# Performance work log

Measured on AMD Instinct MI355X. Metric: run time of the kernel, lower is better.

Reference implementation:

```python
import jax, jax.numpy as jnp
import numpy as np

H = 1024
V_IN = 32000
V_OUT = 32000
T = 2048
BOS, EOS = 1, 2
MAX_STEPS = 50


def setup_inputs() -> dict:
    key = jax.random.key(0)
    ks = jax.random.split(key, 10)
    def n(k, shape, scale=0.05):
        return jax.random.normal(k, shape, jnp.float32) * scale
    return {
        "src_ids": jax.random.randint(ks[0], (T,), 3, V_IN),
        "embed_input": n(ks[1], (V_IN, H), 0.1),
        "We_ih": n(ks[2], (4 * H, H)),
        "We_hh": n(ks[3], (4 * H, H)),
        "be": jnp.zeros((4 * H,), jnp.float32),
        "embed_target": n(ks[4], (V_OUT, H), 0.1),
        "Wd_ih": n(ks[5], (4 * H, H)),
        "Wd_hh": n(ks[6], (4 * H, H)),
        "bd": jnp.zeros((4 * H,), jnp.float32),
        "W_attn": n(ks[7], (H, 2 * H)),
        "b_attn": jnp.zeros((H,), jnp.float32),
        "W_out": n(ks[8], (V_OUT, H)),
        "b_out": jnp.zeros((V_OUT,), jnp.float32),
    }


def _lstm_cell(x, h, c, W_ih, W_hh, b):
    # torch LSTMCell gate order: i, f, g, o (b = b_ih + b_hh folded)
    g = W_ih @ x + W_hh @ h + b  # [4H]
    i, f, gg, o = jnp.split(g, 4)
    i = jax.nn.sigmoid(i)
    f = jax.nn.sigmoid(f)
    o = jax.nn.sigmoid(o)
    gg = jnp.tanh(gg)
    c2 = f * c + i * gg
    return o * jnp.tanh(c2), c2


def reference(src_ids, embed_input, We_ih, We_hh, be, embed_target,
              Wd_ih, Wd_hh, bd, W_attn, b_attn, W_out, b_out):
    # ---- encoder: token-wise LSTMCell scan (batch 1, state squeezed to [H]) ----
    emb = embed_input[src_ids]  # [T, H] gather (unknown-word fallback handled by in-range ids)
    h0 = jnp.zeros((H,), jnp.float32)

    def enc_step(carry, x):
        h, c = carry
        h, c = _lstm_cell(x, h, c, We_ih, We_hh, be)
        return (h, c), h

    (hT, cT), hs = jax.lax.scan(enc_step, (h0, h0), emb)  # hs: [T, H]

    # ---- greedy decoder with dot attention, fixed 50 steps + done mask ----
    def dec_step(carry, _):
        wid, ht, ct, done = carry
        x = embed_target[wid]
        ht, ct = _lstm_cell(x, ht, ct, Wd_ih, Wd_hh, bd)
        a = jax.nn.softmax(hs @ ht)          # [T] attention over encoder states
        d = a @ hs                           # [H] context
        ht_new = jnp.tanh(W_attn @ jnp.concatenate([d, ht]) + b_attn)
        logits = W_out @ ht_new + b_out      # [V_OUT]; softmax before argmax is monotone -> skip
        nid = jnp.argmax(logits).astype(wid.dtype)
        tok = jnp.where(done, 0, nid)        # pad after <eos>
        out_logits = jnp.where(done, 0.0, logits)
        done2 = done | (nid == EOS)
        return (nid, ht, ct, done2), (tok, out_logits)

    init = (jnp.asarray(BOS, src_ids.dtype), hT, cT, jnp.asarray(False))
    _, (tokens, logits) = jax.lax.scan(dec_step, init, None, length=MAX_STEPS)
    return tokens, logits  # [50], [50, V_OUT]
```

## Files before the change

### kernel.cpp

```cpp
#include <hip/hip_runtime.h>
#include <hip/hip_cooperative_groups.h>
#include <math.h>

#define HD     1024
#define TLEN   2048
#define G4H    4096
#define VOUTN  32000
#define NSTEP  50
#define BOS_ID 1
#define EOS_ID 2

#define NBLK   256
#define NTHR   256
#define JPB    (HD / NBLK)
#define TPB    (TLEN / NBLK)
#define NBLK_L 500
#define RPW_L  16

#define ENBLK 64
#define ENTHR 1024
#define EJPB  (HD / ENBLK)

#define SENTINEL 0xFFFFFFFFu

#define OFF_GX   ((size_t)0)
#define OFF_HS   (OFF_GX + (size_t)TLEN * G4H)
#define OFF_HD   (OFF_HS + (size_t)(TLEN + 1) * HD)
#define OFF_SC   (OFF_HD + 2 * HD)
#define OFF_DC   (OFF_SC + TLEN)
#define OFF_HTN  (OFF_DC + HD)
#define OFF_BMV  (OFF_HTN + HD)
#define OFF_BMI  (OFF_BMV + 512)
#define OFF_CT   (OFF_BMI + 512)
#define OFF_ST   (OFF_CT + HD)
#define OFF_HST  (OFF_ST + 64)
#define WS_NEED_HST ((OFF_HST + (size_t)HD * TLEN) * sizeof(float))

#define DEV_SCOPE __HIP_MEMORY_SCOPE_AGENT

__device__ __forceinline__ float dload(const float* p) {
    return __hip_atomic_load(p, __ATOMIC_RELAXED, DEV_SCOPE);
}
__device__ __forceinline__ void dstore(float* p, float v) {
    __hip_atomic_store(p, v, __ATOMIC_RELAXED, DEV_SCOPE);
}

__global__ __launch_bounds__(256) void fill_sentinel(float* __restrict__ hsrow1)
{
    const size_t i = ((size_t)blockIdx.x * 256 + threadIdx.x) * 4;
    uint4 v = make_uint4(SENTINEL, SENTINEL, SENTINEL, SENTINEL);
    *(uint4*)(hsrow1 + i) = v;
}

__global__ __launch_bounds__(256) void gx_gemm(
    const int* __restrict__ src_ids,
    const float* __restrict__ emb,
    const float* __restrict__ Wih,
    const float* __restrict__ be,
    float* __restrict__ Gx)
{
    __shared__ float As[128][17];
    __shared__ float Bs[128][17];
    __shared__ int   sid[128];

    const int tid = threadIdx.x;
    const int t0 = blockIdx.x * 128;
    const int r0 = blockIdx.y * 128;

    if (tid < 128) sid[tid] = src_ids[t0 + tid];
    __syncthreads();

    const int tx = tid & 15;
    const int ty = tid >> 4;
    const int lrow = tid >> 1;
    const int lk   = (tid & 1) * 8;

    float acc[8][8];
#pragma unroll
    for (int i = 0; i < 8; ++i)
#pragma unroll
        for (int j = 0; j < 8; ++j) acc[i][j] = 0.f;

    for (int k0 = 0; k0 < HD; k0 += 16) {
        {
            const float* xa = emb + (size_t)sid[lrow] * HD + k0 + lk;
            float4 v0 = *(const float4*)xa;
            float4 v1 = *(const float4*)(xa + 4);
            As[lrow][lk + 0] = v0.x; As[lrow][lk + 1] = v0.y;
            As[lrow][lk + 2] = v0.z; As[lrow][lk + 3] = v0.w;
            As[lrow][lk + 4] = v1.x; As[lrow][lk + 5] = v1.y;
            As[lrow][lk + 6] = v1.z; As[lrow][lk + 7] = v1.w;
            const float* wb = Wih + (size_t)(r0 + lrow) * HD + k0 + lk;
            float4 w0 = *(const float4*)wb;
            float4 w1 = *(const float4*)(wb + 4);
            Bs[lrow][lk + 0] = w0.x; Bs[lrow][lk + 1] = w0.y;
            Bs[lrow][lk + 2] = w0.z; Bs[lrow][lk + 3] = w0.w;
            Bs[lrow][lk + 4] = w1.x; Bs[lrow][lk + 5] = w1.y;
            Bs[lrow][lk + 6] = w1.z; Bs[lrow][lk + 7] = w1.w;
        }
        __syncthreads();
#pragma unroll
        for (int kk = 0; kk < 16; ++kk) {
            float a[8], bv[8];
#pragma unroll
            for (int i = 0; i < 8; ++i) a[i]  = As[ty * 8 + i][kk];
#pragma unroll
            for (int j = 0; j < 8; ++j) bv[j] = Bs[tx * 8 + j][kk];
#pragma unroll
            for (int i = 0; i < 8; ++i)
#pragma unroll
                for (int j = 0; j < 8; ++j)
                    acc[i][j] = fmaf(a[i], bv[j], acc[i][j]);
        }
        __syncthreads();
    }

    float bev[8];
#pragma unroll
    for (int j = 0; j < 8; ++j) bev[j] = be[r0 + tx * 8 + j];
#pragma unroll
    for (int i = 0; i < 8; ++i) {
        const int t = t0 + ty * 8 + i;
        float* dst = Gx + (size_t)t * G4H + r0 + tx * 8;
#pragma unroll
        for (int j = 0; j < 8; ++j) dst[j] = acc[i][j] + bev[j];
    }
}

__global__ __launch_bounds__(1024, 4) void enc_kernel(
    const float* __restrict__ Whh,
    const float* __restrict__ Gx,
    float* __restrict__ wsf)
{
    float* hs   = wsf + OFF_HS;
    float* hd   = wsf + OFF_HD;
    float* cdec = wsf + OFF_CT;
    int*   st   = (int*)(wsf + OFF_ST);

    const int b    = blockIdx.x;
    const int tid  = threadIdx.x;
    const int w    = tid >> 6;
    const int lane = tid & 63;
    const int j0   = b * EJPB;
    const int g    = w >> 2;
    const int e0   = (w & 3) * 4;

    __shared__ float bufH[HD];
    __shared__ float g_s[64];
    __shared__ float c_s[EJPB];
    __shared__ float gxbuf[64];

    float wreg[4][16];
#pragma unroll
    for (int d = 0; d < 4; ++d) {
        const int grow = g * HD + j0 + e0 + d;
        const float* src = Whh + (size_t)grow * HD + lane;
#pragma unroll
        for (int q = 0; q < 16; ++q) wreg[d][q] = src[q * 64];
    }

    if (tid < EJPB) c_s[tid] = 0.f;

    for (int t = 0; t < TLEN; ++t) {
        {
            const float* src = hs + (size_t)t * HD + tid;
            float v = dload(src);
            while (__float_as_uint(v) == SENTINEL) {
                __builtin_amdgcn_s_sleep(1);
                v = dload(src);
            }
            bufH[tid] = v;
        }
        __syncthreads();

        if (tid >= 64 && tid < 128) {
            const int idx = tid - 64;
            const int gg2 = idx >> 4;
            const int ee  = idx & 15;
            gxbuf[idx] = Gx[(size_t)t * G4H + gg2 * HD + j0 + ee];
        }

        float acc[4];
#pragma unroll
        for (int d = 0; d < 4; ++d) {
            float a = 0.f;
#pragma unroll
            for (int q = 0; q < 16; ++q)
                a = fmaf(wreg[d][q], bufH[q * 64 + lane], a);
#pragma unroll
            for (int off = 32; off > 0; off >>= 1) a += __shfl_down(a, off);
            acc[d] = a;
        }
        if (lane == 0) {
#pragma unroll
            for (int d = 0; d < 4; ++d) g_s[g * 16 + e0 + d] = acc[d];
        }
        __syncthreads();

        if (tid < EJPB) {
            const int j = j0 + tid;
            const float gi = g_s[tid]      + gxbuf[tid];
            const float gf = g_s[16 + tid] + gxbuf[16 + tid];
            const float gg = g_s[32 + tid] + gxbuf[32 + tid];
            const float go = g_s[48 + tid] + gxbuf[48 + tid];
            const float i_ = 1.f / (1.f + expf(-gi));
            const float f_ = 1.f / (1.f + expf(-gf));
            const float o_ = 1.f / (1.f + expf(-go));
            const float g2 = tanhf(gg);
            const float c2 = f_ * c_s[tid] + i_ * g2;
            c_s[tid] = c2;
            dstore(hs + (size_t)(t + 1) * HD + j, o_ * tanhf(c2));
        }
    }

    if (tid < EJPB) {
        cdec[j0 + tid] = c_s[tid];
        hd[j0 + tid]   = hs[(size_t)TLEN * HD + j0 + tid];
    }
    if (b == 0 && tid == 0) st[0] = BOS_ID;
}

__global__ __launch_bounds__(256) void k_transpose(
    const float* __restrict__ hs, float* __restrict__ hsT)
{
    __shared__ float tile[32][33];
    const int t0  = blockIdx.x * 32;
    const int j0b = blockIdx.y * 32;
    const int tx  = threadIdx.x & 31;
    const int ty  = threadIdx.x >> 5;
#pragma unroll
    for (int k = 0; k < 4; ++k) {
        const int trow = t0 + ty + k * 8;
        tile[ty + k * 8][tx] = hs[(size_t)(trow + 1) * HD + j0b + tx];
    }
    __syncthreads();
#pragma unroll
    for (int k = 0; k < 4; ++k) {
        const int j = j0b + ty + k * 8;
        hsT[(size_t)j * TLEN + t0 + tx] = tile[tx][ty + k * 8];
    }
}

__global__ __launch_bounds__(256) void k_gates(
    const float* __restrict__ embT,
    const float* __restrict__ Wdih,
    const float* __restrict__ Wdhh,
    const float* __restrict__ bdv,
    float* __restrict__ wsf,
    float* __restrict__ out, int s)
{
    float* hd   = wsf + OFF_HD;
    float* cdec = wsf + OFF_CT;
    int*   st   = (int*)(wsf + OFF_ST);
    const float* bmv = wsf + OFF_BMV;
    const int*   bmi = (const int*)(wsf + OFF_BMI);

    const int b    = blockIdx.x;
    const int tid  = threadIdx.x;
    const int w    = tid >> 6;
    const int lane = tid & 63;
    const int j0   = b * JPB;

    const float* hcur = hd + (s & 1) * HD;
    float*       hnxt = hd + ((s + 1) & 1) * HD;

    __shared__ float bufAB[2 * HD];
    __shared__ float g_s[4 * JPB];
    __shared__ float rv[NTHR];
    __shared__ int   ri[NTHR];
    __shared__ int   s_wid;

    for (int i = tid; i < HD; i += NTHR) bufAB[HD + i] = hcur[i];

    if (s == 0) {
        if (tid == 0) s_wid = st[0] & 0xFFFF;
        __syncthreads();
    } else {
        float v1 = bmv[tid]; int i1 = bmi[tid];
        if (tid + 256 < NBLK_L) {
            float v2 = bmv[tid + 256]; int i2 = bmi[tid + 256];
            if (v2 > v1 || (v2 == v1 && i2 < i1)) { v1 = v2; i1 = i2; }
        }
        rv[tid] = v1; ri[tid] = i1;
        __syncthreads();
        for (int s2 = 128; s2 > 0; s2 >>= 1) {
            if (tid < s2) {
                if (rv[tid + s2] > rv[tid] ||
                    (rv[tid + s2] == rv[tid] && ri[tid + s2] < ri[tid])) {
                    rv[tid] = rv[tid + s2]; ri[tid] = ri[tid + s2];
                }
            }
            __syncthreads();
        }
        if (tid == 0) {
            const int nid   = ri[0];
            const int prev  = st[s - 1];
            const int dprev = (prev >> 16) & 1;
            const int dnew  = dprev | (nid == EOS_ID);
            s_wid = nid;
            if (b == 0) {
                out[s - 1] = dprev ? 0.f : (float)nid;
                st[s] = (dnew << 16) | nid;
            }
        }
        __syncthreads();
    }

    const float* x = embT + (size_t)s_wid * HD;
    for (int i = tid; i < HD; i += NTHR) bufAB[i] = x[i];
    __syncthreads();

    const float4* buf4 = (const float4*)bufAB;
#pragma unroll
    for (int d = 0; d < 4; ++d) {
        const int grow = w * HD + j0 + d;
        const float4* wi4 = (const float4*)(Wdih + (size_t)grow * HD);
        const float4* wh4 = (const float4*)(Wdhh + (size_t)grow * HD);
        float4 a4 = make_float4(0.f, 0.f, 0.f, 0.f);
#pragma unroll
        for (int q = 0; q < 4; ++q) {
            float4 wv = wi4[q * 64 + lane], xv = buf4[q * 64 + lane];
            a4.x = fmaf(wv.x, xv.x, a4.x); a4.y = fmaf(wv.y, xv.y, a4.y);
            a4.z = fmaf(wv.z, xv.z, a4.z); a4.w = fmaf(wv.w, xv.w, a4.w);
            float4 wv2 = wh4[q * 64 + lane], hv = buf4[256 + q * 64 + lane];
            a4.x = fmaf(wv2.x, hv.x, a4.x); a4.y = fmaf(wv2.y, hv.y, a4.y);
            a4.z = fmaf(wv2.z, hv.z, a4.z); a4.w = fmaf(wv2.w, hv.w, a4.w);
        }
        float a = (a4.x + a4.y) + (a4.z + a4.w);
#pragma unroll
        for (int off = 32; off > 0; off >>= 1) a += __shfl_down(a, off);
        if (lane == 0) g_s[w * 4 + d] = a;
    }
    __syncthreads();

    if (tid < JPB) {
        const int j = j0 + tid;
        const float gi = g_s[0 * 4 + tid] + bdv[0 * HD + j];
        const float gf = g_s[1 * 4 + tid] + bdv[1 * HD + j];
        const float gg = g_s[2 * 4 + tid] + bdv[2 * HD + j];
        const float go = g_s[3 * 4 + tid] + bdv[3 * HD + j];
        const float i_ = 1.f / (1.f + expf(-gi));
        const float f_ = 1.f / (1.f + expf(-gf));
        const float o_ = 1.f / (1.f + expf(-go));
        const float g2 = tanhf(gg);
        const float c2 = f_ * cdec[j] + i_ * g2;
        cdec[j] = c2;
        hnxt[j] = o_ * tanhf(c2);
    }
}

__global__ __launch_bounds__(256) void k_scores(float* __restrict__ wsf, int s)
{
    const float* hs = wsf + OFF_HS;
    const float* hnxt = wsf + OFF_HD + (size_t)((s + 1) & 1) * HD;
    float* sc = wsf + OFF_SC;

    const int b    = blockIdx.x;
    const int tid  = threadIdx.x;
    const int w    = tid >> 6;
    const int lane = tid & 63;

    __shared__ float bufH[HD];
    const float4* buf4 = (const float4*)bufH;
    for (int i = tid; i < HD; i += NTHR) bufH[i] = hnxt[i];
    __syncthreads();

#pragma unroll
    for (int d = 0; d < 2; ++d) {
        const int t = b * TPB + w * 2 + d;
        const float4* hr4 = (const float4*)(hs + (size_t)(t + 1) * HD);
        float4 a4 = make_float4(0.f, 0.f, 0.f, 0.f);
#pragma unroll
        for (int q = 0; q < 4; ++q) {
            float4 hv = hr4[q * 64 + lane], bv = buf4[q * 64 + lane];
            a4.x = fmaf(hv.x, bv.x, a4.x); a4.y = fmaf(hv.y, bv.y, a4.y);
            a4.z = fmaf(hv.z, bv.z, a4.z); a4.w = fmaf(hv.w, bv.w, a4.w);
        }
        float a = (a4.x + a4.y) + (a4.z + a4.w);
#pragma unroll
        for (int off = 32; off > 0; off >>= 1) a += __shfl_down(a, off);
        if (lane == 0) sc[t] = a;
    }
}

__global__ __launch_bounds__(256) void k_ctx(
    float* __restrict__ wsf, const float* __restrict__ hsT)
{
    const float* hs = wsf + OFF_HS;
    const float* sc = wsf + OFF_SC;
    float* dctx = wsf + OFF_DC;

    const int b    = blockIdx.x;
    const int tid  = threadIdx.x;
    const int w    = tid >> 6;
    const int lane = tid & 63;
    const int j0   = b * JPB;

    __shared__ float sc_s[TLEN];
    __shared__ float red[NTHR];

    for (int t = tid; t < TLEN; t += NTHR) sc_s[t] = sc[t];
    __syncthreads();

    float lm = -INFINITY;
    for (int t = tid; t < TLEN; t += NTHR) lm = fmaxf(lm, sc_s[t]);
    red[tid] = lm; __syncthreads();
    for (int s2 = NTHR / 2; s2 > 0; s2 >>= 1) {
        if (tid < s2) red[tid] = fmaxf(red[tid], red[tid + s2]);
        __syncthreads();
    }
    const float m = red[0]; __syncthreads();
    float lz = 0.f;
    for (int t = tid; t < TLEN; t += NTHR) lz += __expf(sc_s[t] - m);
    red[tid] = lz; __syncthreads();
    for (int s2 = NTHR / 2; s2 > 0; s2 >>= 1) {
        if (tid < s2) red[tid] += red[tid + s2];
        __syncthreads();
    }
    const float Zi = 1.f / red[0]; __syncthreads();

    const int j = j0 + w;
    float a = 0.f;
    if (hsT) {
        const float* row = hsT + (size_t)j * TLEN;
#pragma unroll
        for (int it = 0; it < TLEN / 64; ++it) {
            const int t = lane + it * 64;
            a = fmaf(__expf(sc_s[t] - m) * Zi, row[t], a);
        }
    } else {
#pragma unroll
        for (int it = 0; it < TLEN / 64; ++it) {
            const int t = lane + it * 64;
            a = fmaf(__expf(sc_s[t] - m) * Zi, hs[(size_t)(t + 1) * HD + j], a);
        }
    }
#pragma unroll
    for (int off = 32; off > 0; off >>= 1) a += __shfl_down(a, off);
    if (lane == 0) dctx[j] = a;
}

__global__ __launch_bounds__(256) void k_attn(
    const float* __restrict__ Wattn,
    const float* __restrict__ battn,
    float* __restrict__ wsf, int s)
{
    const float* dctx = wsf + OFF_DC;
    const float* hnxt = wsf + OFF_HD + (size_t)((s + 1) & 1) * HD;
    float* htn = wsf + OFF_HTN;

    const int b    = blockIdx.x;
    const int tid  = threadIdx.x;
    const int w    = tid >> 6;
    const int lane = tid & 63;
    const int j0   = b * JPB;

    __shared__ float bufAB[2 * HD];
    const float4* buf4 = (const float4*)bufAB;
    for (int i = tid; i < HD; i += NTHR) {
        bufAB[i]      = dctx[i];
        bufAB[HD + i] = hnxt[i];
    }
    __syncthreads();

    const int j = j0 + w;
    const float4* wr4 = (const float4*)(Wattn + (size_t)j * (2 * HD));
    float4 a4 = make_float4(0.f, 0.f, 0.f, 0.f);
#pragma unroll
    for (int q = 0; q < 8; ++q) {
        float4 wv = wr4[q * 64 + lane], bv = buf4[q * 64 + lane];
        a4.x = fmaf(wv.x, bv.x, a4.x); a4.y = fmaf(wv.y, bv.y, a4.y);
        a4.z = fmaf(wv.z, bv.z, a4.z); a4.w = fmaf(wv.w, bv.w, a4.w);
    }
    float a = (a4.x + a4.y) + (a4.z + a4.w);
#pragma unroll
    for (int off = 32; off > 0; off >>= 1) a += __shfl_down(a, off);
    if (lane == 0) htn[j] = tanhf(a + battn[j]);
}

__global__ __launch_bounds__(256) void k_logits(
    const float* __restrict__ Wout,
    const float* __restrict__ bout,
    float* __restrict__ wsf,
    float* __restrict__ out, int s)
{
    const float* htn = wsf + OFF_HTN;
    float* bmv = wsf + OFF_BMV;
    int*   bmi = (int*)(wsf + OFF_BMI);
    const int* st = (const int*)(wsf + OFF_ST);

    const int b    = blockIdx.x;
    const int tid  = threadIdx.x;
    const int w    = tid >> 6;
    const int lane = tid & 63;

    __shared__ float bufH[HD];
    __shared__ float red[4];
    __shared__ int   redi[4];
    const float4* buf4 = (const float4*)bufH;

    const int donev = (st[s] >> 16) & 1;
    for (int i = tid; i < HD; i += NTHR) bufH[i] = htn[i];
    __syncthreads();

    const int rbeg = b * 64 + w * RPW_L;
    float bv = -INFINITY; int bi = 0x7fffffff;
    for (int r = rbeg; r < rbeg + RPW_L; r += 2) {
        const float4* w0 = (const float4*)(Wout + (size_t)r * HD);
        const float4* w1 = (const float4*)(Wout + (size_t)(r + 1) * HD);
        float4 a04 = make_float4(0.f, 0.f, 0.f, 0.f);
        float4 a14 = make_float4(0.f, 0.f, 0.f, 0.f);
#pragma unroll
        for (int q = 0; q < 4; ++q) {
            float4 hv = buf4[q * 64 + lane];
            float4 x0 = w0[q * 64 + lane];
            float4 x1 = w1[q * 64 + lane];
            a04.x = fmaf(x0.x, hv.x, a04.x); a04.y = fmaf(x0.y, hv.y, a04.y);
            a04.z = fmaf(x0.z, hv.z, a04.z); a04.w = fmaf(x0.w, hv.w, a04.w);
            a14.x = fmaf(x1.x, hv.x, a14.x); a14.y = fmaf(x1.y, hv.y, a14.y);
            a14.z = fmaf(x1.z, hv.z, a14.z); a14.w = fmaf(x1.w, hv.w, a14.w);
        }
        float a0 = (a04.x + a04.y) + (a04.z + a04.w);
        float a1 = (a14.x + a14.y) + (a14.z + a14.w);
#pragma unroll
        for (int off = 32; off > 0; off >>= 1) {
            a0 += __shfl_down(a0, off);
            a1 += __shfl_down(a1, off);
        }
        if (lane == 0) {
            a0 += bout[r];
            a1 += bout[r + 1];
            out[NSTEP + (size_t)s * VOUTN + r]     = donev ? 0.f : a0;
            out[NSTEP + (size_t)s * VOUTN + r + 1] = donev ? 0.f : a1;
            if (a0 > bv) { bv = a0; bi = r; }
            if (a1 > bv) { bv = a1; bi = r + 1; }
        }
    }
    if (lane == 0) { red[w] = bv; redi[w] = bi; }
    __syncthreads();
    if (tid == 0) {
        float v = red[0]; int ii = redi[0];
#pragma unroll
        for (int q = 1; q < 4; ++q)
            if (red[q] > v || (red[q] == v && redi[q] < ii)) { v = red[q]; ii = redi[q]; }
        bmv[b] = v; bmi[b] = ii;
    }
}

__global__ __launch_bounds__(256) void k_amax_final(
    float* __restrict__ wsf, float* __restrict__ out)
{
    const float* bmv = wsf + OFF_BMV;
    const int*   bmi = (const int*)(wsf + OFF_BMI);
    const int*   st  = (const int*)(wsf + OFF_ST);

    const int tid = threadIdx.x;
    __shared__ float red[NTHR];
    __shared__ int   redi[NTHR];

    float v1 = bmv[tid]; int i1 = bmi[tid];
    if (tid + 256 < NBLK_L) {
        float v2 = bmv[tid + 256]; int i2 = bmi[tid + 256];
        if (v2 > v1 || (v2 == v1 && i2 < i1)) { v1 = v2; i1 = i2; }
    }
    red[tid] = v1; redi[tid] = i1;
    __syncthreads();
    for (int s2 = 128; s2 > 0; s2 >>= 1) {
        if (tid < s2) {
            if (red[tid + s2] > red[tid] ||
                (red[tid + s2] == red[tid] && redi[tid + s2] < redi[tid])) {
                red[tid] = red[tid + s2]; redi[tid] = redi[tid + s2];
            }
        }
        __syncthreads();
    }
    if (tid == 0) {
        const int nid   = redi[0];
        const int donev = (st[NSTEP - 1] >> 16) & 1;
        out[NSTEP - 1] = donev ? 0.f : (float)nid;
    }
}

extern "C" void kernel_launch(void* const* d_in, const int* in_sizes, int n_in,
                              void* d_out, int out_size, void* d_ws, size_t ws_size,
                              hipStream_t stream) {
    (void)in_sizes; (void)n_in; (void)out_size;
    const int*   src_ids = (const int*)  d_in[0];
    const float* emb_in  = (const float*)d_in[1];
    const float* We_ih   = (const float*)d_in[2];
    const float* We_hh   = (const float*)d_in[3];
    const float* be      = (const float*)d_in[4];
    const float* emb_tgt = (const float*)d_in[5];
    const float* Wd_ih   = (const float*)d_in[6];
    const float* Wd_hh   = (const float*)d_in[7];
    const float* bd      = (const float*)d_in[8];
    const float* W_attn  = (const float*)d_in[9];
    const float* b_attn  = (const float*)d_in[10];
    const float* W_out   = (const float*)d_in[11];
    const float* b_out   = (const float*)d_in[12];

    float* outp = (float*)d_out;
    float* wsf  = (float*)d_ws;

    const bool use_hsT = (ws_size >= WS_NEED_HST);
    const float* hsTp = use_hsT ? (wsf + OFF_HST) : nullptr;

    hipMemsetAsync(wsf + OFF_HS, 0, HD * sizeof(float), stream);
    fill_sentinel<<<TLEN, 256, 0, stream>>>(wsf + OFF_HS + HD);

    dim3 g1(TLEN / 128, G4H / 128);
    gx_gemm<<<g1, 256, 0, stream>>>(src_ids, emb_in, We_ih, be, wsf + OFF_GX);

    {
        const float* a_Whh = We_hh;
        const float* a_Gx  = wsf + OFF_GX;
        float* a_ws  = wsf;
        void* args[] = { &a_Whh, &a_Gx, &a_ws };
        hipLaunchCooperativeKernel(reinterpret_cast<void*>(enc_kernel),
                                   dim3(ENBLK), dim3(ENTHR), args, 0, stream);
    }

    if (use_hsT)
        k_transpose<<<dim3(TLEN / 32, HD / 32), 256, 0, stream>>>(
            wsf + OFF_HS, wsf + OFF_HST);

    for (int s = 0; s < NSTEP; ++s) {
        k_gates <<<NBLK,   NTHR, 0, stream>>>(emb_tgt, Wd_ih, Wd_hh, bd, wsf, outp, s);
        k_scores<<<NBLK,   NTHR, 0, stream>>>(wsf, s);
        k_ctx   <<<NBLK,   NTHR, 0, stream>>>(wsf, hsTp);
        k_attn  <<<NBLK,   NTHR, 0, stream>>>(W_attn, b_attn, wsf, s);
        k_logits<<<NBLK_L, NTHR, 0, stream>>>(W_out, b_out, wsf, outp, s);
    }
    k_amax_final<<<1, NTHR, 0, stream>>>(wsf, outp);
}
```

Before: 8.522 ms.

## Precompute W_attn·hs projection and fuse context with attention; register-load encoder h

Precomputes P = W_attn[:, :H] @ hs^T once after the encoder, so each decoder step computes the context term as softmax weights times rows of P instead of a separate context kernel followed by the attention matvec. The ctx and attn kernels are merged into one launch per step, which removes one launch and one global round trip per step. The encoder also loads h directly into registers with a contiguous per-lane layout and a wave-wide sentinel poll, replacing the shared-memory staging and one __syncthreads. The cost is an extra 1024x2048x1024 GEMM up front, and per-step contiguous 16-float loads per lane that may coalesce worse.

```diff
diff --git a/kernel.cpp b/kernel.cpp
--- a/kernel.cpp
+++ b/kernel.cpp
@@ -33,8 +33,8 @@
 #define OFF_BMI  (OFF_BMV + 512)
 #define OFF_CT   (OFF_BMI + 512)
 #define OFF_ST   (OFF_CT + HD)
-#define OFF_HST  (OFF_ST + 64)
-#define WS_NEED_HST ((OFF_HST + (size_t)HD * TLEN) * sizeof(float))
+#define OFF_P    (OFF_ST + 64)
+#define WS_NEED_P ((OFF_P + (size_t)HD * TLEN) * sizeof(float))
 
 #define DEV_SCOPE __HIP_MEMORY_SCOPE_AGENT
 
@@ -139,14 +139,13 @@
 
     const int b    = blockIdx.x;
     const int tid  = threadIdx.x;
+    const int lane = tid & 63;
     const int w    = tid >> 6;
-    const int lane = tid & 63;
     const int j0   = b * EJPB;
     const int g    = w >> 2;
     const int e0   = (w & 3) * 4;
 
-    __shared__ float bufH[HD];
-    __shared__ float g_s[64];
+    __shared__ float g_s[2][64];
     __shared__ float c_s[EJPB];
     __shared__ float gxbuf[64];
 
@@ -154,30 +153,34 @@
 #pragma unroll
     for (int d = 0; d < 4; ++d) {
         const int grow = g * HD + j0 + e0 + d;
-        const float* src = Whh + (size_t)grow * HD + lane;
-#pragma unroll
-        for (int q = 0; q < 16; ++q) wreg[d][q] = src[q * 64];
+        const float* src = Whh + (size_t)grow * HD + lane * 16;
+#pragma unroll
+        for (int q = 0; q < 16; ++q) wreg[d][q] = src[q];
     }
 
     if (tid < EJPB) c_s[tid] = 0.f;
+    __syncthreads();
 
     for (int t = 0; t < TLEN; ++t) {
-        {
-            const float* src = hs + (size_t)t * HD + tid;
-            float v = dload(src);
-            while (__float_as_uint(v) == SENTINEL) {
-                __builtin_amdgcn_s_sleep(1);
-                v = dload(src);
-            }
-            bufH[tid] = v;
-        }
-        __syncthreads();
+        float hreg[16];
+        const float* hrow = hs + (size_t)t * HD + lane * 16;
+#pragma unroll
+        for (int q = 0; q < 16; ++q) hreg[q] = dload(hrow + q);
+        for (;;) {
+            bool bad = false;
+#pragma unroll
+            for (int q = 0; q < 16; ++q)
+                bad = bad || (__float_as_uint(hreg[q]) == SENTINEL);
+            if (!__any(bad)) break;
+            __builtin_amdgcn_s_sleep(1);
+#pragma unroll
+            for (int q = 0; q < 16; ++q)
+                if (__float_as_uint(hreg[q]) == SENTINEL) hreg[q] = dload(hrow + q);
+        }
 
         if (tid >= 64 && tid < 128) {
             const int idx = tid - 64;
-            const int gg2 = idx >> 4;
-            const int ee  = idx & 15;
-            gxbuf[idx] = Gx[(size_t)t * G4H + gg2 * HD + j0 + ee];
+            gxbuf[idx] = Gx[(size_t)t * G4H + (idx >> 4) * HD + j0 + (idx & 15)];
         }
 
         float acc[4];
@@ -185,24 +188,23 @@
         for (int d = 0; d < 4; ++d) {
             float a = 0.f;
 #pragma unroll
-            for (int q = 0; q < 16; ++q)
-                a = fmaf(wreg[d][q], bufH[q * 64 + lane], a);
+            for (int q = 0; q < 16; ++q) a = fmaf(wreg[d][q], hreg[q], a);
 #pragma unroll
             for (int off = 32; off > 0; off >>= 1) a += __shfl_down(a, off);
             acc[d] = a;
         }
         if (lane == 0) {
 #pragma unroll
-            for (int d = 0; d < 4; ++d) g_s[g * 16 + e0 + d] = acc[d];
+            for (int d = 0; d < 4; ++d) g_s[t & 1][g * 16 + e0 + d] = acc[d];
         }
         __syncthreads();
 
         if (tid < EJPB) {
             const int j = j0 + tid;
-            const float gi = g_s[tid]      + gxbuf[tid];
-            const float gf = g_s[16 + tid] + gxbuf[16 + tid];
-            const float gg = g_s[32 + tid] + gxbuf[32 + tid];
-            const float go = g_s[48 + tid] + gxbuf[48 + tid];
+            const float gi = g_s[t & 1][tid]      + gxbuf[tid];
+            const float gf = g_s[t & 1][16 + tid] + gxbuf[16 + tid];
+            const float gg = g_s[t & 1][32 + tid] + gxbuf[32 + tid];
+            const float go = g_s[t & 1][48 + tid] + gxbuf[48 + tid];
             const float i_ = 1.f / (1.f + expf(-gi));
             const float f_ = 1.f / (1.f + expf(-gf));
             const float o_ = 1.f / (1.f + expf(-go));
@@ -220,24 +222,67 @@
     if (b == 0 && tid == 0) st[0] = BOS_ID;
 }
 
-__global__ __launch_bounds__(256) void k_transpose(
-    const float* __restrict__ hs, float* __restrict__ hsT)
-{
-    __shared__ float tile[32][33];
-    const int t0  = blockIdx.x * 32;
-    const int j0b = blockIdx.y * 32;
-    const int tx  = threadIdx.x & 31;
-    const int ty  = threadIdx.x >> 5;
-#pragma unroll
-    for (int k = 0; k < 4; ++k) {
-        const int trow = t0 + ty + k * 8;
-        tile[ty + k * 8][tx] = hs[(size_t)(trow + 1) * HD + j0b + tx];
-    }
-    __syncthreads();
-#pragma unroll
-    for (int k = 0; k < 4; ++k) {
-        const int j = j0b + ty + k * 8;
-        hsT[(size_t)j * TLEN + t0 + tx] = tile[tx][ty + k * 8];
+__global__ __launch_bounds__(256) void p_gemm(
+    const float* __restrict__ Wattn,
+    const float* __restrict__ hs,
+    float* __restrict__ P)
+{
+    __shared__ float As[128][17];
+    __shared__ float Bs[128][17];
+
+    const int tid = threadIdx.x;
+    const int j0 = blockIdx.x * 128;
+    const int t0 = blockIdx.y * 128;
+    const int tx = tid & 15;
+    const int ty = tid >> 4;
+    const int lrow = tid >> 1;
+    const int lk   = (tid & 1) * 8;
+
+    float acc[8][8];
+#pragma unroll
+    for (int i = 0; i < 8; ++i)
+#pragma unroll
+        for (int j = 0; j < 8; ++j) acc[i][j] = 0.f;
+
+    for (int k0 = 0; k0 < HD; k0 += 16) {
+        {
+            const float* wa = Wattn + (size_t)(j0 + lrow) * (2 * HD) + k0 + lk;
+            float4 v0 = *(const float4*)wa;
+            float4 v1 = *(const float4*)(wa + 4);
+            As[lrow][lk + 0] = v0.x; As[lrow][lk + 1] = v0.y;
+            As[lrow][lk + 2] = v0.z; As[lrow][lk + 3] = v0.w;
+            As[lrow][lk + 4] = v1.x; As[lrow][lk + 5] = v1.y;
+            As[lrow][lk + 6] = v1.z; As[lrow][lk + 7] = v1.w;
+            const float* hb = hs + (size_t)(t0 + lrow + 1) * HD + k0 + lk;
+            float4 h0 = *(const float4*)hb;
+            float4 h1 = *(const float4*)(hb + 4);
+            Bs[lrow][lk + 0] = h0.x; Bs[lrow][lk + 1] = h0.y;
+            Bs[lrow][lk + 2] = h0.z; Bs[lrow][lk + 3] = h0.w;
+            Bs[lrow][lk + 4] = h1.x; Bs[lrow][lk + 5] = h1.y;
+            Bs[lrow][lk + 6] = h1.z; Bs[lrow][lk + 7] = h1.w;
+        }
+        __syncthreads();
+#pragma unroll
+        for (int kk = 0; kk < 16; ++kk) {
+            float a[8], bv[8];
+#pragma unroll
+            for (int i = 0; i < 8; ++i) a[i]  = As[ty * 8 + i][kk];
+#pragma unroll
+            for (int j = 0; j < 8; ++j) bv[j] = Bs[tx * 8 + j][kk];
+#pragma unroll
+            for (int i = 0; i < 8; ++i)
+#pragma unroll
+                for (int j = 0; j < 8; ++j)
+                    acc[i][j] = fmaf(a[i], bv[j], acc[i][j]);
+        }
+        __syncthreads();
+    }
+
+#pragma unroll
+    for (int i = 0; i < 8; ++i) {
+        float* dst = P + (size_t)(j0 + ty * 8 + i) * TLEN + t0 + tx * 8;
+#pragma unroll
+        for (int j = 0; j < 8; ++j) dst[j] = acc[i][j];
     }
 }
 
@@ -383,12 +428,15 @@
     }
 }
 
-__global__ __launch_bounds__(256) void k_ctx(
-    float* __restrict__ wsf, const float* __restrict__ hsT)
-{
-    const float* hs = wsf + OFF_HS;
+__global__ __launch_bounds__(256) void k_ctxattn(
+    const float* __restrict__ Wattn,
+    const float* __restrict__ battn,
+    float* __restrict__ wsf,
+    const float* __restrict__ P, int s)
+{
     const float* sc = wsf + OFF_SC;
-    float* dctx = wsf + OFF_DC;
+    const float* hnxt = wsf + OFF_HD + (size_t)((s + 1) & 1) * HD;
+    float* htn = wsf + OFF_HTN;
 
     const int b    = blockIdx.x;
     const int tid  = threadIdx.x;
@@ -397,9 +445,11 @@
     const int j0   = b * JPB;
 
     __shared__ float sc_s[TLEN];
+    __shared__ float bufH[HD];
     __shared__ float red[NTHR];
 
     for (int t = tid; t < TLEN; t += NTHR) sc_s[t] = sc[t];
+    for (int i = tid; i < HD; i += NTHR) bufH[i] = hnxt[i];
     __syncthreads();
 
     float lm = -INFINITY;
@@ -421,19 +471,68 @@
 
     const int j = j0 + w;
     float a = 0.f;
-    if (hsT) {
-        const float* row = hsT + (size_t)j * TLEN;
-#pragma unroll
-        for (int it = 0; it < TLEN / 64; ++it) {
-            const int t = lane + it * 64;
-            a = fmaf(__expf(sc_s[t] - m) * Zi, row[t], a);
-        }
-    } else {
-#pragma unroll
-        for (int it = 0; it < TLEN / 64; ++it) {
-            const int t = lane + it * 64;
-            a = fmaf(__expf(sc_s[t] - m) * Zi, hs[(size_t)(t + 1) * HD + j], a);
-        }
+    const float* Pr = P + (size_t)j * TLEN;
+#pragma unroll
+    for (int it = 0; it < TLEN / 64; ++it) {
+        const int t = lane + it * 64;
+        a = fmaf(__expf(sc_s[t] - m) * Zi, Pr[t], a);
+    }
+    const float4* wr4 = (const float4*)(Wattn + (size_t)j * (2 * HD) + HD);
+    const float4* buf4 = (const float4*)bufH;
+    float4 a4 = make_float4(0.f, 0.f, 0.f, 0.f);
+#pragma unroll
+    for (int q = 0; q < 4; ++q) {
+        float4 wv = wr4[q * 64 + lane], hv = buf4[q * 64 + lane];
+        a4.x = fmaf(wv.x, hv.x, a4.x); a4.y = fmaf(wv.y, hv.y, a4.y);
+        a4.z = fmaf(wv.z, hv.z, a4.z); a4.w = fmaf(wv.w, hv.w, a4.w);
+    }
+    a += (a4.x + a4.y) + (a4.z + a4.w);
+#pragma unroll
+    for (int off = 32; off > 0; off >>= 1) a += __shfl_down(a, off);
+    if (lane == 0) htn[j] = tanhf(a + battn[j]);
+}
+
+__global__ __launch_bounds__(256) void k_ctx_fb(float* __restrict__ wsf)
+{
+    const float* hs = wsf + OFF_HS;
+    const float* sc = wsf + OFF_SC;
+    float* dctx = wsf + OFF_DC;
+
+    const int b    = blockIdx.x;
+    const int tid  = threadIdx.x;
+    const int w    = tid >> 6;
+    const int lane = tid & 63;
+    const int j0   = b * JPB;
+
+    __shared__ float sc_s[TLEN];
+    __shared__ float red[NTHR];
+
+    for (int t = tid; t < TLEN; t += NTHR) sc_s[t] = sc[t];
+    __syncthreads();
+
+    float lm = -INFINITY;
+    for (int t = tid; t < TLEN; t += NTHR) lm = fmaxf(lm, sc_s[t]);
+    red[tid] = lm; __syncthreads();
+    for (int s2 = NTHR / 2; s2 > 0; s2 >>= 1) {
+        if (tid < s2) red[tid] = fmaxf(red[tid], red[tid + s2]);
+        __syncthreads();
+    }
+    const float m = red[0]; __syncthreads();
+    float lz = 0.f;
+    for (int t = tid; t < TLEN; t += NTHR) lz += __expf(sc_s[t] - m);
+    red[tid] = lz; __syncthreads();
+    for (int s2 = NTHR / 2; s2 > 0; s2 >>= 1) {
+        if (tid < s2) red[tid] += red[tid + s2];
+        __syncthreads();
+    }
+    const float Zi = 1.f / red[0]; __syncthreads();
+
+    const int j = j0 + w;
+    float a = 0.f;
+#pragma unroll
+    for (int it = 0; it < TLEN / 64; ++it) {
+        const int t = lane + it * 64;
+        a = fmaf(__expf(sc_s[t] - m) * Zi, hs[(size_t)(t + 1) * HD + j], a);
     }
 #pragma unroll
     for (int off = 32; off > 0; off >>= 1) a += __shfl_down(a, off);
@@ -602,8 +701,7 @@
     float* outp = (float*)d_out;
     float* wsf  = (float*)d_ws;
 
-    const bool use_hsT = (ws_size >= WS_NEED_HST);
-    const float* hsTp = use_hsT ? (wsf + OFF_HST) : nullptr;
+    const bool use_P = (ws_size >= WS_NEED_P);
 
     hipMemsetAsync(wsf + OFF_HS, 0, HD * sizeof(float), stream);
     fill_sentinel<<<TLEN, 256, 0, stream>>>(wsf + OFF_HS + HD);
@@ -620,15 +718,19 @@
                                    dim3(ENBLK), dim3(ENTHR), args, 0, stream);
     }
 
-    if (use_hsT)
-        k_transpose<<<dim3(TLEN / 32, HD / 32), 256, 0, stream>>>(
-            wsf + OFF_HS, wsf + OFF_HST);
+    if (use_P)
+        p_gemm<<<dim3(HD / 128, TLEN / 128), 256, 0, stream>>>(
+            W_attn, wsf + OFF_HS, wsf + OFF_P);
 
     for (int s = 0; s < NSTEP; ++s) {
         k_gates <<<NBLK,   NTHR, 0, stream>>>(emb_tgt, Wd_ih, Wd_hh, bd, wsf, outp, s);
         k_scores<<<NBLK,   NTHR, 0, stream>>>(wsf, s);
-        k_ctx   <<<NBLK,   NTHR, 0, stream>>>(wsf, hsTp);
-        k_attn  <<<NBLK,   NTHR, 0, stream>>>(W_attn, b_attn, wsf, s);
+        if (use_P) {
+            k_ctxattn<<<NBLK, NTHR, 0, stream>>>(W_attn, b_attn, wsf, wsf + OFF_P, s);
+        } else {
+            k_ctx_fb<<<NBLK, NTHR, 0, stream>>>(wsf);
+            k_attn  <<<NBLK, NTHR, 0, stream>>>(W_attn, b_attn, wsf, s);
+        }
         k_logits<<<NBLK_L, NTHR, 0, stream>>>(W_out, b_out, wsf, outp, s);
     }
     k_amax_final<<<1, NTHR, 0, stream>>>(wsf, outp);
```

Result: slower. 24.33 ms (+185.5%).
